# Optimization experiments

Measured on AMD Instinct MI355X. Metric: run time of the kernel, lower is better.

## Reference

```python
import jax, jax.numpy as jnp
import numpy as np

B, S, H, NH, NKV, HD, F, E, TOPK = 2, 1024, 2048, 16, 4, 128, 4096, 8, 2
ROPE_THETA = 1e6
EPS = 1e-5


def _ln(x, w, b):
    mu = jnp.mean(x, -1, keepdims=True)
    var = jnp.mean(jnp.square(x - mu), -1, keepdims=True)
    return (x - mu) * jax.lax.rsqrt(var + EPS) * w + b


def _rotate_half(x):
    h = x.shape[-1] // 2
    return jnp.concatenate([-x[..., h:], x[..., :h]], -1)


def setup_inputs() -> dict:
    key = jax.random.key(0)
    ks = jax.random.split(key, 10)
    s = 0.02
    return {
        "hidden_states": jax.random.normal(ks[0], (B, S, H), jnp.float32),
        "attention_mask": jnp.ones((B, S), jnp.int32),
        "position_ids": jnp.broadcast_to(jnp.arange(S, dtype=jnp.int32), (B, S)),
        "ln1_w": jnp.ones((H,), jnp.float32),
        "ln1_b": jnp.zeros((H,), jnp.float32),
        "ln2_w": jnp.ones((H,), jnp.float32),
        "ln2_b": jnp.zeros((H,), jnp.float32),
        "wq": jax.random.normal(ks[1], (H, NH * HD), jnp.float32) * s,
        "bq": jnp.zeros((NH * HD,), jnp.float32),
        "wk": jax.random.normal(ks[2], (H, NKV * HD), jnp.float32) * s,
        "bk": jnp.zeros((NKV * HD,), jnp.float32),
        "wv": jax.random.normal(ks[3], (H, NKV * HD), jnp.float32) * s,
        "bv": jnp.zeros((NKV * HD,), jnp.float32),
        "wo": jax.random.normal(ks[4], (NH * HD, H), jnp.float32) * s,
        "bo": jnp.zeros((H,), jnp.float32),
        "gate_w": jax.random.normal(ks[5], (H, E), jnp.float32) * s,
        "w1": jax.random.normal(ks[6], (E, H, F), jnp.float32) * s,
        "w2": jax.random.normal(ks[7], (E, F, H), jnp.float32) * s,
        "w3": jax.random.normal(ks[8], (E, H, F), jnp.float32) * s,
    }


def reference(hidden_states, attention_mask, position_ids, ln1_w, ln1_b, ln2_w, ln2_b,
              wq, bq, wk, bk, wv, bv, wo, bo, gate_w, w1, w2, w3):
    b, s, _ = hidden_states.shape
    # --- norm + self-attention + residual ---
    x = _ln(hidden_states, ln1_w, ln1_b)
    q = (x @ wq + bq).reshape(b, s, NH, HD)
    k = (x @ wk + bk).reshape(b, s, NKV, HD)
    v = (x @ wv + bv).reshape(b, s, NKV, HD)
    # rotary embeddings
    inv_freq = 1.0 / (ROPE_THETA ** (jnp.arange(0, HD, 2, dtype=jnp.float32) / HD))
    freqs = position_ids.astype(jnp.float32)[..., None] * inv_freq  # [b,s,HD/2]
    emb = jnp.concatenate([freqs, freqs], -1)                        # [b,s,HD]
    cos = jnp.cos(emb)[:, :, None, :]
    sin = jnp.sin(emb)[:, :, None, :]
    q = q * cos + _rotate_half(q) * sin
    k = k * cos + _rotate_half(k) * sin
    # GQA: repeat kv heads
    rep = NH // NKV
    k = jnp.repeat(k, rep, axis=2)
    v = jnp.repeat(v, rep, axis=2)
    scores = jnp.einsum('bqhd,bkhd->bhqk', q, k) / jnp.sqrt(jnp.float32(HD))
    causal = jnp.tril(jnp.ones((s, s), bool))
    mask = causal[None, None, :, :] & (attention_mask > 0)[:, None, None, :]
    scores = jnp.where(mask, scores, jnp.finfo(scores.dtype).min)
    probs = jax.nn.softmax(scores, -1)
    attn = jnp.einsum('bhqk,bkhd->bqhd', probs, v).reshape(b, s, NH * HD)
    h = hidden_states + (attn @ wo + bo)
    # --- norm + sparse MoE + residual ---
    x2 = _ln(h, ln2_w, ln2_b).reshape(b * s, H)
    logits = x2 @ gate_w                                  # [T,E]
    top_vals, top_idx = jax.lax.top_k(logits, TOPK)
    tw = jax.nn.softmax(top_vals, -1)                     # top-2 routing weights
    T = b * s
    dense_w = jnp.zeros((T, E), x2.dtype).at[jnp.arange(T)[:, None], top_idx].set(tw)
    h1 = jnp.einsum('th,ehf->etf', x2, w1)
    h3 = jnp.einsum('th,ehf->etf', x2, w3)
    eo = jnp.einsum('etf,efh->eth', jax.nn.silu(h1) * h3, w2)
    moe = jnp.einsum('eth,te->th', eo, dense_w)
    return h + moe.reshape(b, s, H)
```

## Files before the change

### kernel.cpp

```cpp
#include <hip/hip_runtime.h>
#include <cmath>

#define LDSK 40

typedef __attribute__((ext_vector_type(4))) float floatx4;
typedef __attribute__((ext_vector_type(8))) short shortx8;
typedef __attribute__((ext_vector_type(4))) short shortx4;

constexpr int cB = 2, cS = 1024, cH = 2048, cNH = 16, cNKV = 4, cHD = 128, cF = 4096;
constexpr int cT = cB * cS;

__device__ __forceinline__ unsigned short f2bf(float f) {
  union { float f; unsigned u; } v; v.f = f;
  unsigned r = v.u + 0x7FFFu + ((v.u >> 16) & 1u);
  return (unsigned short)(r >> 16);
}
__device__ __forceinline__ shortx4 f2bf4(float a, float b, float c, float d) {
  shortx4 s;
  s.x = (short)f2bf(a); s.y = (short)f2bf(b);
  s.z = (short)f2bf(c); s.w = (short)f2bf(d);
  return s;
}

template <int EPI>
__global__ __launch_bounds__(256) void gemm32(const float* __restrict__ A,
                                              const float* __restrict__ B,
                                              float* __restrict__ C,
                                              const float* __restrict__ bias,
                                              const float* __restrict__ resid,
                                              int K, long lda, long ldb, long ldc) {
  __shared__ __align__(16) float As[16][68];
  __shared__ __align__(16) float Bs[16][68];
  int tid = threadIdx.x;
  int m0 = blockIdx.y * 64, n0 = blockIdx.x * 64;
  float acc[4][4] = {};
  int ty = tid >> 4, tx = tid & 15;
  for (int k0 = 0; k0 < K; k0 += 16) {
#pragma unroll
    for (int it = 0; it < 4; ++it) {
      int idx = tid + it * 256;
      int m = idx >> 4, k = idx & 15;
      As[k][m] = A[(long)(m0 + m) * lda + k0 + k];
      int n = idx & 63, kb = idx >> 6;
      Bs[kb][n] = B[(long)(k0 + kb) * ldb + n0 + n];
    }
    __syncthreads();
#pragma unroll
    for (int k = 0; k < 16; ++k) {
      float4 av = *(const float4*)&As[k][ty * 4];
      float4 bv = *(const float4*)&Bs[k][tx * 4];
      float a4[4] = {av.x, av.y, av.z, av.w};
      float b4[4] = {bv.x, bv.y, bv.z, bv.w};
#pragma unroll
      for (int i = 0; i < 4; ++i)
#pragma unroll
        for (int j = 0; j < 4; ++j) acc[i][j] += a4[i] * b4[j];
    }
    __syncthreads();
  }
#pragma unroll
  for (int i = 0; i < 4; ++i)
#pragma unroll
    for (int j = 0; j < 4; ++j) {
      int gr = m0 + ty * 4 + i, gc = n0 + tx * 4 + j;
      float val = acc[i][j];
      if (EPI >= 1) val += bias[gc];
      if (EPI == 2) val += resid[(long)gr * ldc + gc];
      C[(long)gr * ldc + gc] = val;
    }
}

__global__ __launch_bounds__(256) void qk32(const float* __restrict__ q,
                                            const float* __restrict__ kx,
                                            float* __restrict__ sc, int b) {
  if ((int)blockIdx.x > (int)blockIdx.y) return;
  int h = blockIdx.z, hk = h >> 2;
  int m0 = blockIdx.y * 64, n0 = blockIdx.x * 64;
  const float* Aq = q + (long)b * cS * (cNH * cHD) + h * cHD + (long)m0 * (cNH * cHD);
  const float* Bk = kx + (long)b * cS * (cNKV * cHD) + hk * cHD + (long)n0 * (cNKV * cHD);
  float* Cb = sc + (long)h * cS * cS;
  __shared__ __align__(16) float As[16][68];
  __shared__ __align__(16) float Bs[16][68];
  int tid = threadIdx.x;
  float acc[4][4] = {};
  int ty = tid >> 4, tx = tid & 15;
  for (int k0 = 0; k0 < cHD; k0 += 16) {
#pragma unroll
    for (int it = 0; it < 4; ++it) {
      int idx = tid + it * 256;
      int r = idx >> 4, k = idx & 15;
      As[k][r] = Aq[(long)r * (cNH * cHD) + k0 + k];
      Bs[k][r] = Bk[(long)r * (cNKV * cHD) + k0 + k];
    }
    __syncthreads();
#pragma unroll
    for (int k = 0; k < 16; ++k) {
      float4 av = *(const float4*)&As[k][ty * 4];
      float4 bv = *(const float4*)&Bs[k][tx * 4];
      float a4[4] = {av.x, av.y, av.z, av.w};
      float b4[4] = {bv.x, bv.y, bv.z, bv.w};
#pragma unroll
      for (int i = 0; i < 4; ++i)
#pragma unroll
        for (int j = 0; j < 4; ++j) acc[i][j] += a4[i] * b4[j];
    }
    __syncthreads();
  }
#pragma unroll
  for (int i = 0; i < 4; ++i)
#pragma unroll
    for (int j = 0; j < 4; ++j)
      Cb[(long)(m0 + ty * 4 + i) * cS + n0 + tx * 4 + j] = acc[i][j];
}

__global__ __launch_bounds__(256) void softmax32(float* __restrict__ sc,
                                                 const int* __restrict__ amask, int b) {
  int row = blockIdx.x;
  int qi = row & (cS - 1);
  float* sr = sc + (long)row * cS;
  int tid = threadIdx.x;
  const float scale = 0.08838834764831845f;
  float4 vv = *(const float4*)(sr + tid * 4);
  float va[4] = {vv.x, vv.y, vv.z, vv.w};
  bool ok[4];
  float mx = -INFINITY;
#pragma unroll
  for (int c = 0; c < 4; ++c) {
    int j = tid * 4 + c;
    ok[c] = (j <= qi) && (amask[b * cS + j] > 0);
    va[c] = ok[c] ? va[c] * scale : -INFINITY;
    mx = fmaxf(mx, va[c]);
  }
#pragma unroll
  for (int off = 32; off; off >>= 1) mx = fmaxf(mx, __shfl_down(mx, off));
  __shared__ float r4[4], s4[4];
  if ((tid & 63) == 0) r4[tid >> 6] = mx;
  __syncthreads();
  mx = fmaxf(fmaxf(r4[0], r4[1]), fmaxf(r4[2], r4[3]));
  float ev[4], sum = 0.f;
#pragma unroll
  for (int c = 0; c < 4; ++c) {
    ev[c] = ok[c] ? expf(va[c] - mx) : 0.f;
    sum += ev[c];
  }
#pragma unroll
  for (int off = 32; off; off >>= 1) sum += __shfl_down(sum, off);
  if ((tid & 63) == 0) s4[tid >> 6] = sum;
  __syncthreads();
  sum = s4[0] + s4[1] + s4[2] + s4[3];
  float inv = 1.f / sum;
  float4 r;
  r.x = ev[0] * inv; r.y = ev[1] * inv; r.z = ev[2] * inv; r.w = ev[3] * inv;
  *(float4*)(sr + tid * 4) = r;
}

__global__ __launch_bounds__(256) void pv32(const float* __restrict__ P,
                                            const float* __restrict__ v,
                                            float* __restrict__ attn, int b) {
  int h = blockIdx.z, hk = h >> 2;
  int m0 = blockIdx.y * 64, n0 = blockIdx.x * 64;
  const float* Pr = P + (long)h * cS * cS + (long)m0 * cS;
  const float* Vb = v + (long)b * cS * (cNKV * cHD) + hk * cHD;
  float* Cb = attn + (long)b * cS * (cNH * cHD) + h * cHD;
  __shared__ __align__(16) float As[16][68];
  __shared__ __align__(16) float Bs[16][68];
  int tid = threadIdx.x;
  float acc[4][4] = {};
  int ty = tid >> 4, tx = tid & 15;
  int kend = m0 + 64;
  for (int k0 = 0; k0 < kend; k0 += 16) {
#pragma unroll
    for (int it = 0; it < 4; ++it) {
      int idx = tid + it * 256;
      int m = idx >> 4, k = idx & 15;
      As[k][m] = Pr[(long)m * cS + k0 + k];
      int n = idx & 63, kb = idx >> 6;
      Bs[kb][n] = Vb[(long)(k0 + kb) * (cNKV * cHD) + n0 + n];
    }
    __syncthreads();
#pragma unroll
    for (int k = 0; k < 16; ++k) {
      float4 av = *(const float4*)&As[k][ty * 4];
      float4 bv = *(const float4*)&Bs[k][tx * 4];
      float a4[4] = {av.x, av.y, av.z, av.w};
      float b4[4] = {bv.x, bv.y, bv.z, bv.w};
#pragma unroll
      for (int i = 0; i < 4; ++i)
#pragma unroll
        for (int j = 0; j < 4; ++j) acc[i][j] += a4[i] * b4[j];
    }
    __syncthreads();
  }
#pragma unroll
  for (int i = 0; i < 4; ++i)
#pragma unroll
    for (int j = 0; j < 4; ++j)
      Cb[(long)(m0 + ty * 4 + i) * (cNH * cHD) + n0 + tx * 4 + j] = acc[i][j];
}

__global__ __launch_bounds__(256) void ln_kernel(const float* __restrict__ in,
                                                 const float* __restrict__ w,
                                                 const float* __restrict__ b,
                                                 float* __restrict__ out) {
  int t = blockIdx.x, tid = threadIdx.x;
  const float* xr = in + (long)t * cH;
  float* yr = out + (long)t * cH;
  float4 v0 = *(const float4*)(xr + tid * 4);
  float4 v1 = *(const float4*)(xr + 1024 + tid * 4);
  float s1 = v0.x + v0.y + v0.z + v0.w + v1.x + v1.y + v1.z + v1.w;
  float s2 = v0.x * v0.x + v0.y * v0.y + v0.z * v0.z + v0.w * v0.w +
             v1.x * v1.x + v1.y * v1.y + v1.z * v1.z + v1.w * v1.w;
#pragma unroll
  for (int off = 32; off; off >>= 1) {
    s1 += __shfl_down(s1, off);
    s2 += __shfl_down(s2, off);
  }
  __shared__ float rs1[4], rs2[4];
  if ((tid & 63) == 0) { rs1[tid >> 6] = s1; rs2[tid >> 6] = s2; }
  __syncthreads();
  float ts1 = rs1[0] + rs1[1] + rs1[2] + rs1[3];
  float ts2 = rs2[0] + rs2[1] + rs2[2] + rs2[3];
  float mu = ts1 * (1.f / 2048.f);
  float var = ts2 * (1.f / 2048.f) - mu * mu;
  float rstd = rsqrtf(var + 1e-5f);
#pragma unroll
  for (int half = 0; half < 2; ++half) {
    int bi = tid * 4 + half * 1024;
    float4 vv = half ? v1 : v0;
    float4 wv4 = *(const float4*)(w + bi);
    float4 bv4 = *(const float4*)(b + bi);
    float4 r;
    r.x = (vv.x - mu) * rstd * wv4.x + bv4.x;
    r.y = (vv.y - mu) * rstd * wv4.y + bv4.y;
    r.z = (vv.z - mu) * rstd * wv4.z + bv4.z;
    r.w = (vv.w - mu) * rstd * wv4.w + bv4.w;
    *(float4*)(yr + bi) = r;
  }
}

__global__ __launch_bounds__(256) void rope_kernel(float* __restrict__ x,
                                                   const int* __restrict__ pos, int nheads) {
  int row = blockIdx.x * 4 + (threadIdx.x >> 6);
  int lane = threadIdx.x & 63;
  int t = row / nheads;
  float* p = x + (long)row * cHD;
  float ang = (float)pos[t] * exp2f(-(float)lane * (19.931568569324174f / 64.f));
  float s, c;
  sincosf(ang, &s, &c);
  float lo = p[lane], hi = p[lane + 64];
  p[lane] = lo * c - hi * s;
  p[lane + 64] = hi * c + lo * s;
}

__global__ void zero_cnt(int* c) {
  if (threadIdx.x < 8) c[threadIdx.x] = 0;
}
__global__ __launch_bounds__(256) void gate_topk(const float* __restrict__ x2,
                                                 const float* __restrict__ gw,
                                                 int* __restrict__ cnt, int* __restrict__ lists,
                                                 float* __restrict__ wsl) {
  int t = blockIdx.x, tid = threadIdx.x;
  const float* xr = x2 + (long)t * cH;
  float a[8] = {0, 0, 0, 0, 0, 0, 0, 0};
  for (int h = tid; h < cH; h += 256) {
    float xv = xr[h];
    float4 g0 = *(const float4*)(gw + h * 8);
    float4 g1 = *(const float4*)(gw + h * 8 + 4);
    a[0] += xv * g0.x; a[1] += xv * g0.y; a[2] += xv * g0.z; a[3] += xv * g0.w;
    a[4] += xv * g1.x; a[5] += xv * g1.y; a[6] += xv * g1.z; a[7] += xv * g1.w;
  }
  __shared__ float red[256 * 8];
#pragma unroll
  for (int e = 0; e < 8; ++e) red[tid * 8 + e] = a[e];
  __syncthreads();
  for (int s = 128; s > 0; s >>= 1) {
    if (tid < s)
#pragma unroll
      for (int e = 0; e < 8; ++e) red[tid * 8 + e] += red[(tid + s) * 8 + e];
    __syncthreads();
  }
  if (tid == 0) {
    float lg[8];
#pragma unroll
    for (int e = 0; e < 8; ++e) lg[e] = red[e];
    int i0 = 0;
#pragma unroll
    for (int e = 1; e < 8; ++e) if (lg[e] > lg[i0]) i0 = e;
    int i1 = -1;
#pragma unroll
    for (int e = 0; e < 8; ++e)
      if (e != i0 && (i1 < 0 || lg[e] > lg[i1])) i1 = e;
    float e1 = expf(lg[i1] - lg[i0]);
    float w0 = 1.f / (1.f + e1);
    float w1 = e1 / (1.f + e1);
    int p0 = atomicAdd(&cnt[i0], 1);
    lists[i0 * cT + p0] = 2 * t;
    int p1 = atomicAdd(&cnt[i1], 1);
    lists[i1 * cT + p1] = 2 * t + 1;
    wsl[2 * t] = w0;
    wsl[2 * t + 1] = w1;
  }
}

__device__ __forceinline__ void stage_rows_f32_gather(short* Sdst, const float* x2,
                                                      const int* ent, int k0, int tid) {
#pragma unroll
  for (int it = 0; it < 4; ++it) {
    int idx = tid + it * 256;
    int m = idx >> 3, c4 = idx & 7;
    float4 v = *(const float4*)(x2 + (long)(ent[m] >> 1) * cH + k0 + c4 * 4);
    *(shortx4*)&Sdst[m * LDSK + c4 * 4] = f2bf4(v.x, v.y, v.z, v.w);
  }
}
__device__ __forceinline__ void stage_rows_bf16_gather(short* Sdst, const short* z,
                                                       const int* ent, long ld, int k0, int tid) {
#pragma unroll
  for (int it = 0; it < 2; ++it) {
    int idx = tid + it * 256;
    int m = idx >> 2, c8 = idx & 3;
    shortx8 v = *(const shortx8*)(z + (long)ent[m] * ld + k0 + c8 * 8);
    *(shortx8*)&Sdst[m * LDSK + c8 * 8] = v;
  }
}
__device__ __forceinline__ void stage_B_kxn(short* Bs, const float* Bm, long ldb,
                                            int n0, int k0, int tid) {
  int n = tid & 127, kg = tid >> 7;
  const float* p = Bm + (long)(k0 + kg * 16) * ldb + n0 + n;
  float v[16];
#pragma unroll
  for (int i = 0; i < 16; ++i) v[i] = p[(long)i * ldb];
#pragma unroll
  for (int w = 0; w < 4; ++w)
    *(shortx4*)&Bs[n * LDSK + kg * 16 + w * 4] =
        f2bf4(v[4 * w], v[4 * w + 1], v[4 * w + 2], v[4 * w + 3]);
}
__device__ __forceinline__ void mfma_step(const short* As, const short* Bs,
                                          floatx4 acc[4][4], int wm, int wn, int lane) {
  int lr = lane & 15, qd = lane >> 4;
  shortx8 af[4], bfr[4];
#pragma unroll
  for (int i = 0; i < 4; ++i)
    af[i] = *(const shortx8*)&As[(wm * 64 + i * 16 + lr) * LDSK + qd * 8];
#pragma unroll
  for (int j = 0; j < 4; ++j)
    bfr[j] = *(const shortx8*)&Bs[(wn * 64 + j * 16 + lr) * LDSK + qd * 8];
#pragma unroll
  for (int i = 0; i < 4; ++i)
#pragma unroll
    for (int j = 0; j < 4; ++j)
      acc[i][j] = __builtin_amdgcn_mfma_f32_16x16x32_bf16(af[i], bfr[j], acc[i][j], 0, 0, 0);
}

__global__ __launch_bounds__(256) void moe_gemm1(const float* __restrict__ x2,
                                                 const float* __restrict__ w1,
                                                 const float* __restrict__ w3,
                                                 const int* __restrict__ cnt,
                                                 const int* __restrict__ lists,
                                                 const float* __restrict__ wsl,
                                                 short* __restrict__ z) {
  int e = blockIdx.z, mt = blockIdx.y, n0 = blockIdx.x * 128;
  int c = cnt[e];
  if (mt * 128 >= c) return;
  __shared__ int ent[128];
  __shared__ float wrt[128];
  int tid = threadIdx.x;
  if (tid < 128) {
    int r = mt * 128 + tid;
    int en = (r < c) ? lists[e * cT + r] : 0;
    ent[tid] = en;
    wrt[tid] = (r < c) ? wsl[en] : 0.f;
  }
  __syncthreads();
  __shared__ __align__(16) short As[128 * LDSK];
  __shared__ __align__(16) short Bs1[128 * LDSK];
  __shared__ __align__(16) short Bs3[128 * LDSK];
  const float* W1 = w1 + (long)e * cH * cF;
  const float* W3 = w3 + (long)e * cH * cF;
  floatx4 a1[4][4] = {}, a3[4][4] = {};
  int lane = tid & 63, wvv = tid >> 6, wm = wvv >> 1, wn = wvv & 1;
  for (int k0 = 0; k0 < cH; k0 += 32) {
    stage_rows_f32_gather(As, x2, ent, k0, tid);
    stage_B_kxn(Bs1, W1, cF, n0, k0, tid);
    stage_B_kxn(Bs3, W3, cF, n0, k0, tid);
    __syncthreads();
    mfma_step(As, Bs1, a1, wm, wn, lane);
    mfma_step(As, Bs3, a3, wm, wn, lane);
    __syncthreads();
  }
  int lr = lane & 15, qd = lane >> 4;
  int rlim = c - mt * 128;
#pragma unroll
  for (int i = 0; i < 4; ++i)
#pragma unroll
    for (int r = 0; r < 4; ++r) {
      int row = wm * 64 + i * 16 + qd * 4 + r;
      if (row < rlim) {
        long zb = (long)ent[row] * cF + n0;
        float wgt = wrt[row];
#pragma unroll
        for (int j = 0; j < 4; ++j) {
          float h1 = a1[i][j][r], h3 = a3[i][j][r];
          float sv = h1 / (1.f + __expf(-h1));
          z[zb + wn * 64 + j * 16 + lr] = (short)f2bf(wgt * sv * h3);
        }
      }
    }
}

__global__ __launch_bounds__(256) void moe_gemm2(const short* __restrict__ z,
                                                 const float* __restrict__ w2,
                                                 const int* __restrict__ cnt,
                                                 const int* __restrict__ lists,
                                                 float* __restrict__ eo) {
  int e = blockIdx.z, mt = blockIdx.y, n0 = blockIdx.x * 128;
  int c = cnt[e];
  if (mt * 128 >= c) return;
  __shared__ int ent[128];
  int tid = threadIdx.x;
  if (tid < 128) {
    int r = mt * 128 + tid;
    ent[tid] = (r < c) ? lists[e * cT + r] : 0;
  }
  __syncthreads();
  __shared__ __align__(16) short As[128 * LDSK];
  __shared__ __align__(16) short Bs[128 * LDSK];
  const float* W2 = w2 + (long)e * cF * cH;
  floatx4 acc[4][4] = {};
  int lane = tid & 63, wvv = tid >> 6, wm = wvv >> 1, wn = wvv & 1;
  for (int k0 = 0; k0 < cF; k0 += 32) {
    stage_rows_bf16_gather(As, z, ent, cF, k0, tid);
    stage_B_kxn(Bs, W2, cH, n0, k0, tid);
    __syncthreads();
    mfma_step(As, Bs, acc, wm, wn, lane);
    __syncthreads();
  }
  int lr = lane & 15, qd = lane >> 4;
  int rlim = c - mt * 128;
#pragma unroll
  for (int i = 0; i < 4; ++i)
#pragma unroll
    for (int r = 0; r < 4; ++r) {
      int row = wm * 64 + i * 16 + qd * 4 + r;
      if (row < rlim) {
        long ob = (long)ent[row] * cH + n0;
#pragma unroll
        for (int j = 0; j < 4; ++j) eo[ob + wn * 64 + j * 16 + lr] = acc[i][j][r];
      }
    }
}

__global__ __launch_bounds__(256) void final_add(const float* __restrict__ h,
                                                 const float* __restrict__ eo,
                                                 float* __restrict__ out) {
  int t = blockIdx.x, tid = threadIdx.x;
  const float* hr = h + (long)t * cH;
  const float* e0 = eo + (long)(2 * t) * cH;
  const float* e1 = eo + (long)(2 * t + 1) * cH;
  float* orow = out + (long)t * cH;
#pragma unroll
  for (int it = 0; it < 2; ++it) {
    int i = tid * 4 + it * 1024;
    float4 a = *(const float4*)(hr + i);
    float4 b = *(const float4*)(e0 + i);
    float4 c = *(const float4*)(e1 + i);
    float4 r;
    r.x = a.x + b.x + c.x;
    r.y = a.y + b.y + c.y;
    r.z = a.z + b.z + c.z;
    r.w = a.w + b.w + c.w;
    *(float4*)(orow + i) = r;
  }
}

extern "C" void kernel_launch(void* const* d_in, const int* in_sizes, int n_in,
                              void* d_out, int out_size, void* d_ws, size_t ws_size,
                              hipStream_t stream) {
  const float* hidden = (const float*)d_in[0];
  const int* amask = (const int*)d_in[1];
  const int* posid = (const int*)d_in[2];
  const float* ln1w = (const float*)d_in[3];
  const float* ln1b = (const float*)d_in[4];
  const float* ln2w = (const float*)d_in[5];
  const float* ln2b = (const float*)d_in[6];
  const float* wq = (const float*)d_in[7];
  const float* bq = (const float*)d_in[8];
  const float* wk = (const float*)d_in[9];
  const float* bk = (const float*)d_in[10];
  const float* wv = (const float*)d_in[11];
  const float* bv = (const float*)d_in[12];
  const float* wo = (const float*)d_in[13];
  const float* bo = (const float*)d_in[14];
  const float* gw = (const float*)d_in[15];
  const float* w1 = (const float*)d_in[16];
  const float* w2 = (const float*)d_in[17];
  const float* w3 = (const float*)d_in[18];
  float* out = (float*)d_out;

  char* ws = (char*)d_ws;
  const size_t MB = 1024 * 1024;
  float* x = (float*)(ws);
  float* q = (float*)(ws + 16 * MB);
  float* k = (float*)(ws + 32 * MB);
  float* v = (float*)(ws + 36 * MB);
  float* sc = (float*)(ws + 40 * MB);
  float* attn = x;
  float* hbuf = q;
  float* x2 = sc;
  short* z = (short*)(ws + 56 * MB);
  float* eo = (float*)(ws + 88 * MB);
  int* cnt = (int*)(ws + 120 * MB);
  int* lists = (int*)(ws + 120 * MB + 256);
  float* wsl = (float*)(ws + 120 * MB + 256 + (size_t)8 * cT * 4);

  dim3 blk(256);

  ln_kernel<<<cT, blk, 0, stream>>>(hidden, ln1w, ln1b, x);
  gemm32<1><<<dim3(32, 32), blk, 0, stream>>>(x, wq, q, bq, nullptr, cH, cH, cNH * cHD, cNH * cHD);
  gemm32<1><<<dim3(8, 32), blk, 0, stream>>>(x, wk, k, bk, nullptr, cH, cH, cNKV * cHD, cNKV * cHD);
  gemm32<1><<<dim3(8, 32), blk, 0, stream>>>(x, wv, v, bv, nullptr, cH, cH, cNKV * cHD, cNKV * cHD);
  rope_kernel<<<(cT * cNH) / 4, blk, 0, stream>>>(q, posid, cNH);
  rope_kernel<<<(cT * cNKV) / 4, blk, 0, stream>>>(k, posid, cNKV);
  for (int b = 0; b < cB; ++b) {
    qk32<<<dim3(16, 16, cNH), blk, 0, stream>>>(q, k, sc, b);
    softmax32<<<cNH * cS, blk, 0, stream>>>(sc, amask, b);
    pv32<<<dim3(2, 16, cNH), blk, 0, stream>>>(sc, v, attn, b);
  }
  gemm32<2><<<dim3(32, 32), blk, 0, stream>>>(attn, wo, hbuf, bo, hidden, cH, cH, cH, cH);
  ln_kernel<<<cT, blk, 0, stream>>>(hbuf, ln2w, ln2b, x2);
  zero_cnt<<<1, 64, 0, stream>>>(cnt);
  gate_topk<<<cT, blk, 0, stream>>>(x2, gw, cnt, lists, wsl);
  moe_gemm1<<<dim3(cF / 128, cT / 128, 8), blk, 0, stream>>>(x2, w1, w3, cnt, lists, wsl, z);
  moe_gemm2<<<dim3(cH / 128, cT / 128, 8), blk, 0, stream>>>(z, w2, cnt, lists, eo);
  final_add<<<cT, blk, 0, stream>>>(hbuf, eo, out);
  (void)in_sizes; (void)n_in; (void)out_size; (void)ws_size;
}
```

Baseline: 2.497 ms.

## Double-buffer LDS and register-prefetch tiles in MoE expert GEMMs

Both MoE grouped GEMM kernels now use double-buffered shared-memory tiles, with the next K-slice prefetched into registers while MFMAs run on the current one. This leaves one barrier per iteration instead of two. The aim is to hide global load latency behind compute. Launch bounds now ask for 2 blocks per CU, which limits registers, and LDS use doubles. Together these risk spills, since gemm1 holds two 64-entry accumulator sets plus the prefetch registers.

```diff
diff --git a/kernel.cpp b/kernel.cpp
--- a/kernel.cpp
+++ b/kernel.cpp
@@ -302,38 +302,6 @@
   }
 }
 
-__device__ __forceinline__ void stage_rows_f32_gather(short* Sdst, const float* x2,
-                                                      const int* ent, int k0, int tid) {
-#pragma unroll
-  for (int it = 0; it < 4; ++it) {
-    int idx = tid + it * 256;
-    int m = idx >> 3, c4 = idx & 7;
-    float4 v = *(const float4*)(x2 + (long)(ent[m] >> 1) * cH + k0 + c4 * 4);
-    *(shortx4*)&Sdst[m * LDSK + c4 * 4] = f2bf4(v.x, v.y, v.z, v.w);
-  }
-}
-__device__ __forceinline__ void stage_rows_bf16_gather(short* Sdst, const short* z,
-                                                       const int* ent, long ld, int k0, int tid) {
-#pragma unroll
-  for (int it = 0; it < 2; ++it) {
-    int idx = tid + it * 256;
-    int m = idx >> 2, c8 = idx & 3;
-    shortx8 v = *(const shortx8*)(z + (long)ent[m] * ld + k0 + c8 * 8);
-    *(shortx8*)&Sdst[m * LDSK + c8 * 8] = v;
-  }
-}
-__device__ __forceinline__ void stage_B_kxn(short* Bs, const float* Bm, long ldb,
-                                            int n0, int k0, int tid) {
-  int n = tid & 127, kg = tid >> 7;
-  const float* p = Bm + (long)(k0 + kg * 16) * ldb + n0 + n;
-  float v[16];
-#pragma unroll
-  for (int i = 0; i < 16; ++i) v[i] = p[(long)i * ldb];
-#pragma unroll
-  for (int w = 0; w < 4; ++w)
-    *(shortx4*)&Bs[n * LDSK + kg * 16 + w * 4] =
-        f2bf4(v[4 * w], v[4 * w + 1], v[4 * w + 2], v[4 * w + 3]);
-}
 __device__ __forceinline__ void mfma_step(const short* As, const short* Bs,
                                           floatx4 acc[4][4], int wm, int wn, int lane) {
   int lr = lane & 15, qd = lane >> 4;
@@ -351,13 +319,13 @@
       acc[i][j] = __builtin_amdgcn_mfma_f32_16x16x32_bf16(af[i], bfr[j], acc[i][j], 0, 0, 0);
 }
 
-__global__ __launch_bounds__(256) void moe_gemm1(const float* __restrict__ x2,
-                                                 const float* __restrict__ w1,
-                                                 const float* __restrict__ w3,
-                                                 const int* __restrict__ cnt,
-                                                 const int* __restrict__ lists,
-                                                 const float* __restrict__ wsl,
-                                                 short* __restrict__ z) {
+__global__ __launch_bounds__(256, 2) void moe_gemm1(const float* __restrict__ x2,
+                                                    const float* __restrict__ w1,
+                                                    const float* __restrict__ w3,
+                                                    const int* __restrict__ cnt,
+                                                    const int* __restrict__ lists,
+                                                    const float* __restrict__ wsl,
+                                                    short* __restrict__ z) {
   int e = blockIdx.z, mt = blockIdx.y, n0 = blockIdx.x * 128;
   int c = cnt[e];
   if (mt * 128 >= c) return;
@@ -371,22 +339,70 @@
     wrt[tid] = (r < c) ? wsl[en] : 0.f;
   }
   __syncthreads();
-  __shared__ __align__(16) short As[128 * LDSK];
-  __shared__ __align__(16) short Bs1[128 * LDSK];
-  __shared__ __align__(16) short Bs3[128 * LDSK];
-  const float* W1 = w1 + (long)e * cH * cF;
-  const float* W3 = w3 + (long)e * cH * cF;
+  __shared__ __align__(16) short As[2][128 * LDSK];
+  __shared__ __align__(16) short Bs1[2][128 * LDSK];
+  __shared__ __align__(16) short Bs3[2][128 * LDSK];
+
+  const float* ap[4];
+#pragma unroll
+  for (int it = 0; it < 4; ++it) {
+    int idx = tid + it * 256;
+    ap[it] = x2 + (long)(ent[idx >> 3] >> 1) * cH + (idx & 7) * 4;
+  }
+  int bn = tid & 127, bkg = tid >> 7;
+  const float* b1p = w1 + (long)e * cH * cF + (long)(bkg * 16) * cF + n0 + bn;
+  const float* b3p = w3 + (long)e * cH * cF + (long)(bkg * 16) * cF + n0 + bn;
+
+  float4 ra[4];
+  float rb1[16], rb3[16];
+
+#define G1_LOAD(k0)                                                        \
+  {                                                                        \
+    _Pragma("unroll") for (int it = 0; it < 4; ++it)                       \
+        ra[it] = *(const float4*)(ap[it] + (k0));                          \
+    _Pragma("unroll") for (int i = 0; i < 16; ++i)                         \
+        rb1[i] = b1p[((k0) + i) * cF];                                     \
+    _Pragma("unroll") for (int i = 0; i < 16; ++i)                         \
+        rb3[i] = b3p[((k0) + i) * cF];                                     \
+  }
+
+#define G1_CVTW(buf)                                                       \
+  {                                                                        \
+    _Pragma("unroll") for (int it = 0; it < 4; ++it) {                     \
+      int idx = tid + it * 256;                                            \
+      int m = idx >> 3, c4 = idx & 7;                                      \
+      *(shortx4*)&As[buf][m * LDSK + c4 * 4] =                             \
+          f2bf4(ra[it].x, ra[it].y, ra[it].z, ra[it].w);                   \
+    }                                                                      \
+    _Pragma("unroll") for (int w = 0; w < 4; ++w)                          \
+        *(shortx4*)&Bs1[buf][bn * LDSK + bkg * 16 + w * 4] =               \
+            f2bf4(rb1[4 * w], rb1[4 * w + 1], rb1[4 * w + 2], rb1[4 * w + 3]); \
+    _Pragma("unroll") for (int w = 0; w < 4; ++w)                          \
+        *(shortx4*)&Bs3[buf][bn * LDSK + bkg * 16 + w * 4] =               \
+            f2bf4(rb3[4 * w], rb3[4 * w + 1], rb3[4 * w + 2], rb3[4 * w + 3]); \
+  }
+
   floatx4 a1[4][4] = {}, a3[4][4] = {};
   int lane = tid & 63, wvv = tid >> 6, wm = wvv >> 1, wn = wvv & 1;
-  for (int k0 = 0; k0 < cH; k0 += 32) {
-    stage_rows_f32_gather(As, x2, ent, k0, tid);
-    stage_B_kxn(Bs1, W1, cF, n0, k0, tid);
-    stage_B_kxn(Bs3, W3, cF, n0, k0, tid);
-    __syncthreads();
-    mfma_step(As, Bs1, a1, wm, wn, lane);
-    mfma_step(As, Bs3, a3, wm, wn, lane);
-    __syncthreads();
-  }
+
+  constexpr int NS = cH / 32;
+  G1_LOAD(0);
+  G1_CVTW(0);
+  G1_LOAD(32);
+  __syncthreads();
+  for (int t = 0; t < NS; ++t) {
+    int buf = t & 1;
+    mfma_step(As[buf], Bs1[buf], a1, wm, wn, lane);
+    mfma_step(As[buf], Bs3[buf], a3, wm, wn, lane);
+    if (t + 1 < NS) {
+      G1_CVTW(buf ^ 1);
+      if (t + 2 < NS) G1_LOAD((t + 2) * 32);
+    }
+    __syncthreads();
+  }
+#undef G1_LOAD
+#undef G1_CVTW
+
   int lr = lane & 15, qd = lane >> 4;
   int rlim = c - mt * 128;
 #pragma unroll
@@ -407,11 +423,11 @@
     }
 }
 
-__global__ __launch_bounds__(256) void moe_gemm2(const short* __restrict__ z,
-                                                 const float* __restrict__ w2,
-                                                 const int* __restrict__ cnt,
-                                                 const int* __restrict__ lists,
-                                                 float* __restrict__ eo) {
+__global__ __launch_bounds__(256, 2) void moe_gemm2(const short* __restrict__ z,
+                                                    const float* __restrict__ w2,
+                                                    const int* __restrict__ cnt,
+                                                    const int* __restrict__ lists,
+                                                    float* __restrict__ eo) {
   int e = blockIdx.z, mt = blockIdx.y, n0 = blockIdx.x * 128;
   int c = cnt[e];
   if (mt * 128 >= c) return;
@@ -422,18 +438,61 @@
     ent[tid] = (r < c) ? lists[e * cT + r] : 0;
   }
   __syncthreads();
-  __shared__ __align__(16) short As[128 * LDSK];
-  __shared__ __align__(16) short Bs[128 * LDSK];
-  const float* W2 = w2 + (long)e * cF * cH;
+  __shared__ __align__(16) short As[2][128 * LDSK];
+  __shared__ __align__(16) short Bs[2][128 * LDSK];
+
+  const short* ap[2];
+#pragma unroll
+  for (int it = 0; it < 2; ++it) {
+    int idx = tid + it * 256;
+    ap[it] = z + (long)ent[idx >> 2] * cF + (idx & 3) * 8;
+  }
+  int bn = tid & 127, bkg = tid >> 7;
+  const float* bp = w2 + (long)e * cF * cH + (long)(bkg * 16) * cH + n0 + bn;
+
+  shortx8 raz[2];
+  float rb[16];
+
+#define G2_LOAD(k0)                                                        \
+  {                                                                        \
+    _Pragma("unroll") for (int it = 0; it < 2; ++it)                       \
+        raz[it] = *(const shortx8*)(ap[it] + (k0));                        \
+    _Pragma("unroll") for (int i = 0; i < 16; ++i)                         \
+        rb[i] = bp[((k0) + i) * cH];                                       \
+  }
+
+#define G2_CVTW(buf)                                                       \
+  {                                                                        \
+    _Pragma("unroll") for (int it = 0; it < 2; ++it) {                     \
+      int idx = tid + it * 256;                                            \
+      int m = idx >> 2, c8 = idx & 3;                                      \
+      *(shortx8*)&As[buf][m * LDSK + c8 * 8] = raz[it];                    \
+    }                                                                      \
+    _Pragma("unroll") for (int w = 0; w < 4; ++w)                          \
+        *(shortx4*)&Bs[buf][bn * LDSK + bkg * 16 + w * 4] =                \
+            f2bf4(rb[4 * w], rb[4 * w + 1], rb[4 * w + 2], rb[4 * w + 3]); \
+  }
+
   floatx4 acc[4][4] = {};
   int lane = tid & 63, wvv = tid >> 6, wm = wvv >> 1, wn = wvv & 1;
-  for (int k0 = 0; k0 < cF; k0 += 32) {
-    stage_rows_bf16_gather(As, z, ent, cF, k0, tid);
-    stage_B_kxn(Bs, W2, cH, n0, k0, tid);
-    __syncthreads();
-    mfma_step(As, Bs, acc, wm, wn, lane);
-    __syncthreads();
-  }
+
+  constexpr int NS = cF / 32;
+  G2_LOAD(0);
+  G2_CVTW(0);
+  G2_LOAD(32);
+  __syncthreads();
+  for (int t = 0; t < NS; ++t) {
+    int buf = t & 1;
+    mfma_step(As[buf], Bs[buf], acc, wm, wn, lane);
+    if (t + 1 < NS) {
+      G2_CVTW(buf ^ 1);
+      if (t + 2 < NS) G2_LOAD((t + 2) * 32);
+    }
+    __syncthreads();
+  }
+#undef G2_LOAD
+#undef G2_CVTW
+
   int lr = lane & 15, qd = lane >> 4;
   int rlim = c - mt * 128;
 #pragma unroll
```

New measurement: 2.195 ms. -12.1%, faster.
